# Kernel optimization log

Hardware: AMD Instinct MI355X
Metric: run time of the kernel (lower is better)

The kernel has to match this reference:

```python
import jax, jax.numpy as jnp
import numpy as np

EPS = 1e-5


def setup_inputs() -> dict:
    key = jax.random.key(0)
    ks = jax.random.split(key, 12)
    B, T, F = 8192, 512, 4
    IN = F + 1          # market features + prev_delta
    H = 32              # lstm hidden
    D1 = 32             # decision mlp width
    s = 0.1
    return {
        "x": jax.random.normal(ks[0], (B, T, F), dtype=jnp.float32),
        # BatchNorm1d (inference mode: running stats)
        "bn_gamma": jnp.ones((IN,), jnp.float32),
        "bn_beta": jnp.zeros((IN,), jnp.float32),
        "bn_mean": jnp.zeros((IN,), jnp.float32),
        "bn_var": jnp.ones((IN,), jnp.float32),
        # LSTMCell params, gate order i,f,g,o (torch convention)
        "W_ih": jax.random.normal(ks[1], (4 * H, IN), jnp.float32) * s,
        "b_ih": jax.random.normal(ks[2], (4 * H,), jnp.float32) * s,
        "W_hh": jax.random.normal(ks[3], (4 * H, H), jnp.float32) * s,
        "b_hh": jax.random.normal(ks[4], (4 * H,), jnp.float32) * s,
        # decision MLP: Linear(H,32) -> ReLU -> Linear(32,1) -> Sigmoid
        "W1": jax.random.normal(ks[5], (D1, H), jnp.float32) * s,
        "b1": jax.random.normal(ks[6], (D1,), jnp.float32) * s,
        "W2": jax.random.normal(ks[7], (1, D1), jnp.float32) * s,
        "b2": jax.random.normal(ks[8], (1,), jnp.float32) * s,
    }


def reference(x, bn_gamma, bn_beta, bn_mean, bn_var,
              W_ih, b_ih, W_hh, b_hh, W1, b1, W2, b2):
    B, T, F = x.shape
    H = W_hh.shape[1]
    inv_std = jax.lax.rsqrt(bn_var + EPS)

    def step(carry, x_t):
        h, c, d = carry                                  # [B,H],[B,H],[B,1]
        z = jnp.concatenate([x_t, d], axis=1)            # [B, F+1]
        z = (z - bn_mean) * inv_std * bn_gamma + bn_beta
        gates = z @ W_ih.T + b_ih + h @ W_hh.T + b_hh    # [B, 4H]
        i, f, g, o = jnp.split(gates, 4, axis=1)
        c = jax.nn.sigmoid(f) * c + jax.nn.sigmoid(i) * jnp.tanh(g)
        h = jax.nn.sigmoid(o) * jnp.tanh(c)
        d = jax.nn.sigmoid(jax.nn.relu(h @ W1.T + b1) @ W2.T + b2)  # [B,1]
        return (h, c, d), d

    init = (jnp.zeros((B, H), x.dtype),
            jnp.zeros((B, H), x.dtype),
            jnp.zeros((B, 1), x.dtype))
    _, deltas = jax.lax.scan(step, init, jnp.swapaxes(x, 0, 1))  # [T,B,1]
    return jnp.swapaxes(deltas, 0, 1)                             # [B,T,1]
```

## Files before the change

kernel.cpp:

```cpp
#include <hip/hip_runtime.h>
#include <math.h>

#define T_STEPS 512
#define NF 4
#define HID 32
#define BN_EPS 1e-5f

typedef float    f32x2 __attribute__((ext_vector_type(2)));
typedef float    f32x4 __attribute__((ext_vector_type(4)));
typedef _Float16 f16x2 __attribute__((ext_vector_type(2)));
typedef _Float16 f16x8 __attribute__((ext_vector_type(8)));

struct F8 { f16x2 p[4]; };

__device__ __forceinline__ f16x2 pk16(float x, float y) {
  return __builtin_bit_cast(f16x2, __builtin_amdgcn_cvt_pkrtz(x, y));
}
__device__ __forceinline__ f16x8 mk8(f16x2 a, f16x2 b, f16x2 c, f16x2 d) {
  F8 f; f.p[0] = a; f.p[1] = b; f.p[2] = c; f.p[3] = d;
  return __builtin_bit_cast(f16x8, f);
}
__device__ __forceinline__ float fsigmoid(float x) {
  return __builtin_amdgcn_rcpf(1.0f + __expf(-x));
}
__device__ __forceinline__ float ftanh(float x) {
  return fmaf(__builtin_amdgcn_rcpf(1.0f + __expf(-2.0f * x)), 2.0f, -1.0f);
}
__device__ __forceinline__ f32x4 mfma16(f16x8 a, f16x8 b, f32x4 c) {
  return __builtin_amdgcn_mfma_f32_16x16x32_f16(a, b, c, 0, 0, 0);
}

__global__ __launch_bounds__(64, 2) void hedge_kernel(
    const float* __restrict__ x,
    const float* __restrict__ bn_g, const float* __restrict__ bn_b,
    const float* __restrict__ bn_m, const float* __restrict__ bn_v,
    const float* __restrict__ W_ih, const float* __restrict__ b_ih,
    const float* __restrict__ W_hh, const float* __restrict__ b_hh,
    const float* __restrict__ W1,   const float* __restrict__ b1,
    const float* __restrict__ W2,   const float* __restrict__ b2,
    float* __restrict__ out)
{
  const int lane = threadIdx.x;
  const int n    = lane & 15;
  const int q    = lane >> 4;
  const int row  = blockIdx.x * 16 + n;

  float scale[5], shift[5];
  #pragma unroll
  for (int f = 0; f < 5; ++f) {
    float s = bn_g[f] * rsqrtf(bn_v[f] + BN_EPS);
    scale[f] = s;
    shift[f] = fmaf(-bn_m[f], s, bn_b[f]);
  }

  const f16x2 zz = {(_Float16)0, (_Float16)0};

  f16x8 Ahh[8];
  #pragma unroll
  for (int g = 0; g < 8; ++g) {
    const float* Wr = &W_hh[(16 * g + n) * HID];
    const f32x4 lo = *(const f32x4*)&Wr[4 * q];
    const f32x4 hi = *(const f32x4*)&Wr[16 + 4 * q];
    Ahh[g] = mk8(pk16(lo.x, lo.y), pk16(lo.z, lo.w),
                 pk16(hi.x, hi.y), pk16(hi.z, hi.w));
  }
  f16x8 Aih[8];
  #pragma unroll
  for (int g = 0; g < 8; ++g) {
    const int r = 16 * g + n;
    const float w0 = W_ih[r * 5 + 0] * scale[0];
    const float w1 = W_ih[r * 5 + 1] * scale[1];
    const float w2 = W_ih[r * 5 + 2] * scale[2];
    const float w3 = W_ih[r * 5 + 3] * scale[3];
    const float w4 = W_ih[r * 5 + 4] * scale[4];
    Aih[g] = mk8(q == 0 ? pk16(w0, w1) : zz,
                 q == 0 ? pk16(w2, w3) : zz,
                 q == 0 ? pk16(w4, 0.f) : zz, zz);
  }
  f32x4 Cb[8];
  #pragma unroll
  for (int g = 0; g < 8; ++g) {
    #pragma unroll
    for (int r2 = 0; r2 < 4; ++r2) {
      const int rr = 16 * g + 4 * q + r2;
      float a = b_ih[rr] + b_hh[rr];
      #pragma unroll
      for (int f = 0; f < 5; ++f) a = fmaf(W_ih[rr * 5 + f], shift[f], a);
      Cb[g][r2] = a;
    }
  }
  f16x8 Aw1[2];
  f32x4 Cb1[2];
  f32x4 W2v[2];
  #pragma unroll
  for (int p = 0; p < 2; ++p) {
    const float* Wr = &W1[(16 * p + n) * HID];
    const f32x4 lo = *(const f32x4*)&Wr[4 * q];
    const f32x4 hi = *(const f32x4*)&Wr[16 + 4 * q];
    Aw1[p] = mk8(pk16(lo.x, lo.y), pk16(lo.z, lo.w),
                 pk16(hi.x, hi.y), pk16(hi.z, hi.w));
    #pragma unroll
    for (int r2 = 0; r2 < 4; ++r2) {
      Cb1[p][r2] = b1[16 * p + 4 * q + r2];
      W2v[p][r2] = W2[16 * p + 4 * q + r2];
    }
  }
  const float b2s = b2[0];

  const float* xrow = x + (size_t)row * (T_STEPS * NF);
  float*       orow = out + (size_t)row * T_STEPS;

  float cst[2][4] = {{0, 0, 0, 0}, {0, 0, 0, 0}};
  float d = 0.0f;
  f16x8 Bh = mk8(zz, zz, zz, zz);
  f32x4 xv = *(const f32x4*)xrow;

  #pragma unroll 1
  for (int t = 0; t < T_STEPS; ++t) {
    const int tn = (t + 1 < T_STEPS) ? t + 1 : t;
    const f32x4 xn = *(const f32x4*)(xrow + tn * NF);

    const f16x8 Bz = mk8(q == 0 ? pk16(xv.x, xv.y) : zz,
                         q == 0 ? pk16(xv.z, xv.w) : zz,
                         q == 0 ? pk16(d, 0.f) : zz, zz);

    f32x4 D[8];
    #pragma unroll
    for (int g = 0; g < 8; ++g)
      D[g] = mfma16(Aih[g], Bz, mfma16(Ahh[g], Bh, Cb[g]));

    float hN[8];
    #pragma unroll
    for (int pp = 0; pp < 2; ++pp) {
      #pragma unroll
      for (int r2 = 0; r2 < 4; ++r2) {
        const float I = fsigmoid(D[0 + pp][r2]);
        const float F = fsigmoid(D[2 + pp][r2]);
        const float G = ftanh(D[4 + pp][r2]);
        const float O = fsigmoid(D[6 + pp][r2]);
        float& c = cst[pp][r2];
        c = fmaf(F, c, I * G);
        hN[pp * 4 + r2] = O * ftanh(c);
      }
    }
    Bh = mk8(pk16(hN[0], hN[1]), pk16(hN[2], hN[3]),
             pk16(hN[4], hN[5]), pk16(hN[6], hN[7]));

    const f32x4 M0 = mfma16(Aw1[0], Bh, Cb1[0]);
    const f32x4 M1 = mfma16(Aw1[1], Bh, Cb1[1]);
    float y = 0.0f;
    #pragma unroll
    for (int r2 = 0; r2 < 4; ++r2) {
      y = fmaf(W2v[0][r2], fmaxf(M0[r2], 0.0f), y);
      y = fmaf(W2v[1][r2], fmaxf(M1[r2], 0.0f), y);
    }
    y += __builtin_bit_cast(float, __builtin_amdgcn_ds_swizzle(
             __builtin_bit_cast(int, y), 0x401F));
    y += __shfl_xor(y, 32);
    d = fsigmoid(y + b2s);

    if (q == 0) orow[t] = d;
    xv = xn;
  }
}

extern "C" void kernel_launch(void* const* d_in, const int* in_sizes, int n_in,
                              void* d_out, int out_size, void* d_ws, size_t ws_size,
                              hipStream_t stream) {
  const float* x    = (const float*)d_in[0];
  const float* bn_g = (const float*)d_in[1];
  const float* bn_b = (const float*)d_in[2];
  const float* bn_m = (const float*)d_in[3];
  const float* bn_v = (const float*)d_in[4];
  const float* W_ih = (const float*)d_in[5];
  const float* b_ih = (const float*)d_in[6];
  const float* W_hh = (const float*)d_in[7];
  const float* b_hh = (const float*)d_in[8];
  const float* W1   = (const float*)d_in[9];
  const float* b1   = (const float*)d_in[10];
  const float* W2   = (const float*)d_in[11];
  const float* b2   = (const float*)d_in[12];
  float* out = (float*)d_out;

  const int B = in_sizes[0] / (T_STEPS * NF);
  const int grid = B / 16;

  hipLaunchKernelGGL(hedge_kernel, dim3(grid), dim3(64), 0, stream,
                     x, bn_g, bn_b, bn_m, bn_v, W_ih, b_ih, W_hh, b_hh,
                     W1, b1, W2, b2, out);
}
```

Measured before the change: 576.0 us.

## Split LSTM gates across four waves with LDS exchange and exp2-folded activations

Each block now runs four wavefronts, one per gate type (i, f, g, o). Each wave computes two gate MFMA tiles, applies its sigmoid or tanh with the log2e scale folded into the weights, and shares the activated values through double-buffered shared memory behind a barrier per step. The decision MLP is reordered so that the previous step's delta enters as a per-row FMA correction rather than an MFMA input, which takes it off the start of the gate computation. This spreads the per-step serial work over more waves, at the cost of a __syncthreads and LDS traffic every timestep, and of redundant MLP work in every wave.

```diff
diff --git a/kernel.cpp b/kernel.cpp
--- a/kernel.cpp
+++ b/kernel.cpp
@@ -5,6 +5,7 @@
 #define NF 4
 #define HID 32
 #define BN_EPS 1e-5f
+#define LOG2E 1.44269504088896340736f
 
 typedef float    f32x2 __attribute__((ext_vector_type(2)));
 typedef float    f32x4 __attribute__((ext_vector_type(4)));
@@ -20,17 +21,19 @@
   F8 f; f.p[0] = a; f.p[1] = b; f.p[2] = c; f.p[3] = d;
   return __builtin_bit_cast(f16x8, f);
 }
+#if __has_builtin(__builtin_amdgcn_exp2f)
+__device__ __forceinline__ float ex2(float x) { return __builtin_amdgcn_exp2f(x); }
+#else
+__device__ __forceinline__ float ex2(float x) { return exp2f(x); }
+#endif
 __device__ __forceinline__ float fsigmoid(float x) {
   return __builtin_amdgcn_rcpf(1.0f + __expf(-x));
 }
-__device__ __forceinline__ float ftanh(float x) {
-  return fmaf(__builtin_amdgcn_rcpf(1.0f + __expf(-2.0f * x)), 2.0f, -1.0f);
-}
 __device__ __forceinline__ f32x4 mfma16(f16x8 a, f16x8 b, f32x4 c) {
   return __builtin_amdgcn_mfma_f32_16x16x32_f16(a, b, c, 0, 0, 0);
 }
 
-__global__ __launch_bounds__(64, 2) void hedge_kernel(
+__global__ __launch_bounds__(256, 2) void hedge_kernel(
     const float* __restrict__ x,
     const float* __restrict__ bn_g, const float* __restrict__ bn_b,
     const float* __restrict__ bn_m, const float* __restrict__ bn_v,
@@ -40,7 +43,11 @@
     const float* __restrict__ W2,   const float* __restrict__ b2,
     float* __restrict__ out)
 {
-  const int lane = threadIdx.x;
+  __shared__ f32x4 sact[2][4][2][4][16];
+
+  const int tid  = threadIdx.x;
+  const int lane = tid & 63;
+  const int w    = tid >> 6;
   const int n    = lane & 15;
   const int q    = lane >> 4;
   const int row  = blockIdx.x * 16 + n;
@@ -53,45 +60,38 @@
     shift[f] = fmaf(-bn_m[f], s, bn_b[f]);
   }
 
+  const float ke = (w == 2) ? -2.0f * LOG2E : -LOG2E;
+  const float aA = (w == 2) ?  2.0f : 1.0f;
+  const float bA = (w == 2) ? -1.0f : 0.0f;
+
   const f16x2 zz = {(_Float16)0, (_Float16)0};
 
-  f16x8 Ahh[8];
-  #pragma unroll
-  for (int g = 0; g < 8; ++g) {
+  f16x8 Ahh[2], Aih[2];
+  f32x4 Cb[2], Wd[2];
+  #pragma unroll
+  for (int pp = 0; pp < 2; ++pp) {
+    const int g = 2 * w + pp;
     const float* Wr = &W_hh[(16 * g + n) * HID];
     const f32x4 lo = *(const f32x4*)&Wr[4 * q];
     const f32x4 hi = *(const f32x4*)&Wr[16 + 4 * q];
-    Ahh[g] = mk8(pk16(lo.x, lo.y), pk16(lo.z, lo.w),
-                 pk16(hi.x, hi.y), pk16(hi.z, hi.w));
-  }
-  f16x8 Aih[8];
-  #pragma unroll
-  for (int g = 0; g < 8; ++g) {
-    const int r = 16 * g + n;
-    const float w0 = W_ih[r * 5 + 0] * scale[0];
-    const float w1 = W_ih[r * 5 + 1] * scale[1];
-    const float w2 = W_ih[r * 5 + 2] * scale[2];
-    const float w3 = W_ih[r * 5 + 3] * scale[3];
-    const float w4 = W_ih[r * 5 + 4] * scale[4];
-    Aih[g] = mk8(q == 0 ? pk16(w0, w1) : zz,
-                 q == 0 ? pk16(w2, w3) : zz,
-                 q == 0 ? pk16(w4, 0.f) : zz, zz);
-  }
-  f32x4 Cb[8];
-  #pragma unroll
-  for (int g = 0; g < 8; ++g) {
+    Ahh[pp] = mk8(pk16(ke * lo.x, ke * lo.y), pk16(ke * lo.z, ke * lo.w),
+                  pk16(ke * hi.x, ke * hi.y), pk16(ke * hi.z, ke * hi.w));
+    const float* Wi = &W_ih[(16 * g + n) * 5];
+    Aih[pp] = mk8(q == 0 ? pk16(ke * Wi[0] * scale[0], ke * Wi[1] * scale[1]) : zz,
+                  q == 0 ? pk16(ke * Wi[2] * scale[2], ke * Wi[3] * scale[3]) : zz,
+                  zz, zz);
     #pragma unroll
     for (int r2 = 0; r2 < 4; ++r2) {
       const int rr = 16 * g + 4 * q + r2;
       float a = b_ih[rr] + b_hh[rr];
       #pragma unroll
       for (int f = 0; f < 5; ++f) a = fmaf(W_ih[rr * 5 + f], shift[f], a);
-      Cb[g][r2] = a;
+      Cb[pp][r2] = ke * a;
+      Wd[pp][r2] = ke * W_ih[rr * 5 + 4] * scale[4];
     }
   }
   f16x8 Aw1[2];
-  f32x4 Cb1[2];
-  f32x4 W2v[2];
+  f32x4 Cb1[2], W2v[2];
   #pragma unroll
   for (int p = 0; p < 2; ++p) {
     const float* Wr = &W1[(16 * p + n) * HID];
@@ -110,8 +110,7 @@
   const float* xrow = x + (size_t)row * (T_STEPS * NF);
   float*       orow = out + (size_t)row * T_STEPS;
 
-  float cst[2][4] = {{0, 0, 0, 0}, {0, 0, 0, 0}};
-  float d = 0.0f;
+  float cst0[4] = {0, 0, 0, 0}, cst1[4] = {0, 0, 0, 0};
   f16x8 Bh = mk8(zz, zz, zz, zz);
   f32x4 xv = *(const f32x4*)xrow;
 
@@ -119,35 +118,15 @@
   for (int t = 0; t < T_STEPS; ++t) {
     const int tn = (t + 1 < T_STEPS) ? t + 1 : t;
     const f32x4 xn = *(const f32x4*)(xrow + tn * NF);
+    const int bsel = t & 1;
 
     const f16x8 Bz = mk8(q == 0 ? pk16(xv.x, xv.y) : zz,
-                         q == 0 ? pk16(xv.z, xv.w) : zz,
-                         q == 0 ? pk16(d, 0.f) : zz, zz);
-
-    f32x4 D[8];
-    #pragma unroll
-    for (int g = 0; g < 8; ++g)
-      D[g] = mfma16(Aih[g], Bz, mfma16(Ahh[g], Bh, Cb[g]));
-
-    float hN[8];
-    #pragma unroll
-    for (int pp = 0; pp < 2; ++pp) {
-      #pragma unroll
-      for (int r2 = 0; r2 < 4; ++r2) {
-        const float I = fsigmoid(D[0 + pp][r2]);
-        const float F = fsigmoid(D[2 + pp][r2]);
-        const float G = ftanh(D[4 + pp][r2]);
-        const float O = fsigmoid(D[6 + pp][r2]);
-        float& c = cst[pp][r2];
-        c = fmaf(F, c, I * G);
-        hN[pp * 4 + r2] = O * ftanh(c);
-      }
-    }
-    Bh = mk8(pk16(hN[0], hN[1]), pk16(hN[2], hN[3]),
-             pk16(hN[4], hN[5]), pk16(hN[6], hN[7]));
-
+                         q == 0 ? pk16(xv.z, xv.w) : zz, zz, zz);
+    f32x4 D0 = mfma16(Aih[0], Bz, mfma16(Ahh[0], Bh, Cb[0]));
+    f32x4 D1 = mfma16(Aih[1], Bz, mfma16(Ahh[1], Bh, Cb[1]));
     const f32x4 M0 = mfma16(Aw1[0], Bh, Cb1[0]);
     const f32x4 M1 = mfma16(Aw1[1], Bh, Cb1[1]);
+
     float y = 0.0f;
     #pragma unroll
     for (int r2 = 0; r2 < 4; ++r2) {
@@ -157,11 +136,56 @@
     y += __builtin_bit_cast(float, __builtin_amdgcn_ds_swizzle(
              __builtin_bit_cast(int, y), 0x401F));
     y += __shfl_xor(y, 32);
-    d = fsigmoid(y + b2s);
-
-    if (q == 0) orow[t] = d;
+    float dl = fsigmoid(y + b2s);
+    dl = t ? dl : 0.0f;
+    if (w == 0 && q == 0 && t) orow[t - 1] = dl;
+
+    f32x4 A0, A1;
+    #pragma unroll
+    for (int r2 = 0; r2 < 4; ++r2) {
+      const float d0 = fmaf(Wd[0][r2], dl, D0[r2]);
+      const float d1 = fmaf(Wd[1][r2], dl, D1[r2]);
+      A0[r2] = fmaf(aA, __builtin_amdgcn_rcpf(1.0f + ex2(d0)), bA);
+      A1[r2] = fmaf(aA, __builtin_amdgcn_rcpf(1.0f + ex2(d1)), bA);
+    }
+
+    sact[bsel][w][0][q][n] = A0;
+    sact[bsel][w][1][q][n] = A1;
+    __syncthreads();
+    const f32x4 Iv0 = sact[bsel][0][0][q][n], Iv1 = sact[bsel][0][1][q][n];
+    const f32x4 Fv0 = sact[bsel][1][0][q][n], Fv1 = sact[bsel][1][1][q][n];
+    const f32x4 Gv0 = sact[bsel][2][0][q][n], Gv1 = sact[bsel][2][1][q][n];
+    const f32x4 Ov0 = sact[bsel][3][0][q][n], Ov1 = sact[bsel][3][1][q][n];
+
+    float hN[8];
+    #pragma unroll
+    for (int r2 = 0; r2 < 4; ++r2) {
+      float cc0 = fmaf(Fv0[r2], cst0[r2], Iv0[r2] * Gv0[r2]);
+      float cc1 = fmaf(Fv1[r2], cst1[r2], Iv1[r2] * Gv1[r2]);
+      cst0[r2] = cc0; cst1[r2] = cc1;
+      const float tc0 = fmaf(2.0f, __builtin_amdgcn_rcpf(1.0f + ex2(-2.0f * LOG2E * cc0)), -1.0f);
+      const float tc1 = fmaf(2.0f, __builtin_amdgcn_rcpf(1.0f + ex2(-2.0f * LOG2E * cc1)), -1.0f);
+      hN[r2]     = Ov0[r2] * tc0;
+      hN[4 + r2] = Ov1[r2] * tc1;
+    }
+    Bh = mk8(pk16(hN[0], hN[1]), pk16(hN[2], hN[3]),
+             pk16(hN[4], hN[5]), pk16(hN[6], hN[7]));
     xv = xn;
   }
+
+  const f32x4 M0 = mfma16(Aw1[0], Bh, Cb1[0]);
+  const f32x4 M1 = mfma16(Aw1[1], Bh, Cb1[1]);
+  float y = 0.0f;
+  #pragma unroll
+  for (int r2 = 0; r2 < 4; ++r2) {
+    y = fmaf(W2v[0][r2], fmaxf(M0[r2], 0.0f), y);
+    y = fmaf(W2v[1][r2], fmaxf(M1[r2], 0.0f), y);
+  }
+  y += __builtin_bit_cast(float, __builtin_amdgcn_ds_swizzle(
+           __builtin_bit_cast(int, y), 0x401F));
+  y += __shfl_xor(y, 32);
+  const float dl = fsigmoid(y + b2s);
+  if (w == 0 && q == 0) orow[T_STEPS - 1] = dl;
 }
 
 extern "C" void kernel_launch(void* const* d_in, const int* in_sizes, int n_in,
@@ -185,7 +209,7 @@
   const int B = in_sizes[0] / (T_STEPS * NF);
   const int grid = B / 16;
 
-  hipLaunchKernelGGL(hedge_kernel, dim3(grid), dim3(64), 0, stream,
+  hipLaunchKernelGGL(hedge_kernel, dim3(grid), dim3(256), 0, stream,
                      x, bn_g, bn_b, bn_m, bn_v, W_ih, b_ih, W_hh, b_hh,
                      W1, b1, W2, b2, out);
 }
```

Result: faster. 558.2 us (-3.1%).
